# Optimization experiments

Hardware: AMD Instinct MI355X
Metric: run time of the kernel (lower is better)

The kernel has to match this reference:

```python
import jax, jax.numpy as jnp
import numpy as np

D_HEAD = 64

def setup_inputs() -> dict:
    key = jax.random.key(0)
    kq, kk, kv, km = jax.random.split(key, 4)
    B, H, S, D = 4, 16, 2048, D_HEAD
    q = jax.random.normal(kq, (B, H, S, D), dtype=jnp.float32)
    k = jax.random.normal(kk, (B, H, S, D), dtype=jnp.float32)
    v = jax.random.normal(kv, (B, H, S, D), dtype=jnp.float32)
    mask = jax.random.randint(km, (B, 1, S, S), 0, 2, dtype=jnp.int32)
    return {"q": q, "k": k, "v": v, "mask": mask}

def reference(q, k, v, mask):
    # scores: [B,H,S,S]
    scores = jnp.einsum('bhqd,bhkd->bhqk', q, k) / jnp.sqrt(jnp.asarray(D_HEAD, q.dtype))
    neg_inf = jnp.asarray(-jnp.inf, scores.dtype)
    scores = jnp.where(mask == 0, neg_inf, scores)
    attn = jax.nn.softmax(scores, axis=-1)
    # dropout is identity in eval mode (deterministic reference)
    return jnp.einsum('bhqk,bhkd->bhqd', attn, v)
```

## Files before the change

kernel.cpp:

```cpp
#include <hip/hip_runtime.h>


constexpr int Bc = 4, Hc = 16, Sc = 2048, Dc = 64;
constexpr int QBLK = 128, KVBLK = 64;
constexpr int NT = Sc / KVBLK;

typedef _Float16 half8 __attribute__((ext_vector_type(8)));
typedef _Float16 half4 __attribute__((ext_vector_type(4)));
typedef _Float16 half2v __attribute__((ext_vector_type(2)));
typedef __fp16  fp16x2 __attribute__((ext_vector_type(2)));
typedef float floatx4 __attribute__((ext_vector_type(4)));

#define GLB(p) ((const __attribute__((address_space(1))) void*)(p))
#define LDSP(p) ((__attribute__((address_space(3))) void*)(p))

union U32F2 { unsigned int u; fp16x2 h; };
union U32H2 { unsigned int u; half2v h; };
union PFRAG { unsigned int u[4]; half8 h; };

__device__ inline float dot2acc(unsigned int pu, float acc) {
#if __has_builtin(__builtin_amdgcn_fdot2)
    U32H2 c; c.u = pu;
    half2v ones2 = { (_Float16)1.0f, (_Float16)1.0f };
    return __builtin_amdgcn_fdot2(c.h, ones2, acc, false);
#else
    U32H2 c; c.u = pu;
    return acc + (float)c.h[0] + (float)c.h[1];
#endif
}

__global__ __launch_bounds__(256) void mask_to_bits(
    const int* __restrict__ M, unsigned long long* __restrict__ W)
{
    size_t i = (size_t)blockIdx.x * 256 + threadIdx.x;
    int v = M[i];
    unsigned long long bal = __ballot(v != 0);
    if ((threadIdx.x & 63) == 0) W[i >> 6] = bal;
}

__global__ __launch_bounds__(256) void mask_to_bytes(
    const int* __restrict__ M, unsigned int* __restrict__ M8)
{
    size_t t = (size_t)blockIdx.x * 256 + threadIdx.x;
    const int4* src = (const int4*)M + t * 4;
    uint4 out;
    unsigned int* o = (unsigned int*)&out;
    #pragma unroll
    for (int w = 0; w < 4; ++w) {
        int4 v = src[w];
        o[w] = (v.x ? 0xFFu : 0u) | (v.y ? 0xFF00u : 0u) |
               (v.z ? 0xFF0000u : 0u) | (v.w ? 0xFF000000u : 0u);
    }
    ((uint4*)M8)[t] = out;
}

__global__ __launch_bounds__(256) void kv_convert_v4(
    const float* __restrict__ Kp, const float* __restrict__ Vp,
    unsigned char* __restrict__ K16, unsigned char* __restrict__ V16)
{
    __shared__ float vlds[64][65];
    const int tid = threadIdx.x;
    const int kt  = blockIdx.x;
    const int bh  = blockIdx.y;
    const int kv0 = kt * 64;
    const float* ksrc = Kp + ((size_t)bh * Sc + kv0) * Dc;
    const float* vsrc = Vp + ((size_t)bh * Sc + kv0) * Dc;
    unsigned char* kdst = K16 + (size_t)bh * Sc * 128 + (size_t)kv0 * 128;
    unsigned char* vdst = V16 + (size_t)bh * Sc * 128 + (size_t)kv0 * 128;

    #pragma unroll
    for (int it = 0; it < 4; ++it) {
        int idx = it * 256 + tid;
        int o   = idx >> 4;
        int d0  = (idx & 15) * 4;
        float4 kval = *(const float4*)(ksrc + o * Dc + d0);
        half4 kh;
        kh[0] = (_Float16)kval.x; kh[1] = (_Float16)kval.y;
        kh[2] = (_Float16)kval.z; kh[3] = (_Float16)kval.w;
        int r = ((o >> 2) & 3) * 16 + ((o >> 4) << 2) + (o & 3);
        *(half4*)(kdst + r * 128 + ((d0 * 2) ^ ((r & 7) << 4))) = kh;

        float4 vval = *(const float4*)(vsrc + o * Dc + d0);
        vlds[o][d0]     = vval.x;
        vlds[o][d0 + 1] = vval.y;
        vlds[o][d0 + 2] = vval.z;
        vlds[o][d0 + 3] = vval.w;
    }
    __syncthreads();
    #pragma unroll
    for (int i = 0; i < 2; ++i) {
        int ch  = i * 256 + tid;
        int l15 = ch & 15;
        int lg  = (ch >> 4) & 3;
        int c   = (ch >> 6) & 1;
        int nd  = ch >> 7;
        int d   = nd * 16 + l15;
        half8 h;
        #pragma unroll
        for (int w = 0; w < 4; ++w) {
            int kvlog = lg * 16 + (2 * c + (w >> 1)) * 4 + (w & 1) * 2;
            h[w * 2]     = (_Float16)vlds[kvlog][d];
            h[w * 2 + 1] = (_Float16)vlds[kvlog + 1][d];
        }
        *(half8*)(vdst + ch * 16) = h;
    }
}

template <int MMODE>
__global__ __launch_bounds__(256) void attn_v10(
    const float* __restrict__ Qp,
    const unsigned char* __restrict__ K16, const unsigned char* __restrict__ V16,
    const unsigned char* __restrict__ M8, const unsigned long long* __restrict__ Wb,
    float* __restrict__ Op)
{
    __shared__ __align__(16) unsigned char lds[49152];

    const int tid  = threadIdx.x;
    const int w    = tid >> 6;
    const int lane = tid & 63;
    const int l15  = lane & 15;
    const int lg   = lane >> 4;

    const int ib      = blockIdx.x;
    const int logical = (ib & 7) * 128 + (ib >> 3);
    const int qt = logical & 15;
    const int bh = logical >> 4;
    const int b  = bh >> 4;
    const int q0 = qt * QBLK + w * 32 + l15;
    const int q1 = q0 + 16;

    const size_t qkv_base = (size_t)bh * Sc * Dc;
    const unsigned char* k16src = K16 + (size_t)bh * Sc * 128;
    const unsigned char* v16src = V16 + (size_t)bh * Sc * 128;
    const unsigned char* mp0 = M8 + (size_t)b * Sc * Sc + (size_t)q0 * Sc + lg * 16;
    const unsigned char* mp1 = mp0 + (size_t)16 * Sc;
    const unsigned long long* wr0 = Wb + ((size_t)b * Sc + q0) * (Sc / 64);
    const unsigned long long* wr1 = Wb + ((size_t)b * Sc + q1) * (Sc / 64);

    const float qscale = 0.125f * 1.44269504088896f;
    half8 qfrag[2][2];
    #pragma unroll
    for (int qg = 0; qg < 2; ++qg) {
        const float* qrow = Qp + qkv_base + (size_t)(qg ? q1 : q0) * Dc;
        #pragma unroll
        for (int c = 0; c < 2; ++c) {
            int d0 = c * 32 + lg * 8;
            float4 qa = *(const float4*)(qrow + d0);
            float4 qb = *(const float4*)(qrow + d0 + 4);
            qfrag[qg][c][0] = (_Float16)(qa.x * qscale);
            qfrag[qg][c][1] = (_Float16)(qa.y * qscale);
            qfrag[qg][c][2] = (_Float16)(qa.z * qscale);
            qfrag[qg][c][3] = (_Float16)(qa.w * qscale);
            qfrag[qg][c][4] = (_Float16)(qb.x * qscale);
            qfrag[qg][c][5] = (_Float16)(qb.y * qscale);
            qfrag[qg][c][6] = (_Float16)(qb.z * qscale);
            qfrag[qg][c][7] = (_Float16)(qb.w * qscale);
        }
    }

    floatx4 o_acc[2][4];
    float   l_run[2] = {0.f, 0.f};
    #pragma unroll
    for (int qg = 0; qg < 2; ++qg)
        #pragma unroll
        for (int n = 0; n < 4; ++n) o_acc[qg][n] = (floatx4)0.f;

    const int ldsOff = (w * 2) * 1024;
    const unsigned char* kg = k16src + ldsOff + lane * 16;
    const unsigned char* vg = v16src + ldsOff + lane * 16;

    uint4 mk[3][2];
    unsigned long long wk[3][2];

    auto STAGE = [&](int slot) {
        __builtin_amdgcn_global_load_lds(GLB(kg),        LDSP(lds + slot * 16384 + ldsOff),               16, 0, 0);
        __builtin_amdgcn_global_load_lds(GLB(kg + 1024), LDSP(lds + slot * 16384 + ldsOff + 1024),        16, 0, 0);
        __builtin_amdgcn_global_load_lds(GLB(vg),        LDSP(lds + slot * 16384 + 8192 + ldsOff),        16, 0, 0);
        __builtin_amdgcn_global_load_lds(GLB(vg + 1024), LDSP(lds + slot * 16384 + 8192 + ldsOff + 1024), 16, 0, 0);
        kg += 8192; vg += 8192;
    };
    auto LOADM = [&](int slot) {
        if (MMODE == 0) {
            mk[slot][0] = *(const uint4*)(mp0); mp0 += KVBLK;
            mk[slot][1] = *(const uint4*)(mp1); mp1 += KVBLK;
        } else {
            wk[slot][0] = *wr0; ++wr0;
            wk[slot][1] = *wr1; ++wr1;
        }
    };

    auto COMP = [&](int j) {
        const unsigned char* kbase = lds + j * 16384;
        const unsigned char* vbase = lds + j * 16384 + 8192;

        floatx4 s[2][4];
        __builtin_amdgcn_s_setprio(1);
        #pragma unroll
        for (int n = 0; n < 4; ++n) {
            const unsigned char* krow = kbase + (n * 16 + l15) * 128;
            half8 kf0 = *(const half8*)(krow + ((lg * 16)      ^ ((l15 & 7) << 4)));
            half8 kf1 = *(const half8*)(krow + ((64 + lg * 16) ^ ((l15 & 7) << 4)));
            floatx4 a0 = __builtin_amdgcn_mfma_f32_16x16x32_f16(kf0, qfrag[0][0], (floatx4)0.f, 0, 0, 0);
            a0 = __builtin_amdgcn_mfma_f32_16x16x32_f16(kf1, qfrag[0][1], a0, 0, 0, 0);
            floatx4 a1 = __builtin_amdgcn_mfma_f32_16x16x32_f16(kf0, qfrag[1][0], (floatx4)0.f, 0, 0, 0);
            a1 = __builtin_amdgcn_mfma_f32_16x16x32_f16(kf1, qfrag[1][1], a1, 0, 0, 0);
            s[0][n] = a0;
            s[1][n] = a1;
        }
        __builtin_amdgcn_s_setprio(0);

        PFRAG pf[2][2];
        #pragma unroll
        for (int qg = 0; qg < 2; ++qg) {
            unsigned int nib16;
            if (MMODE == 1) {
                unsigned long long wc = wk[j][qg];
                unsigned int lo = (unsigned int)wc, hi = (unsigned int)(wc >> 32);
                unsigned int half = (lg & 2) ? hi : lo;
                nib16 = (lg & 1) ? (half >> 16) : (half & 0xFFFFu);
            }
            const unsigned int* mw = (const unsigned int*)&mk[j][qg];
            float rs = l_run[qg];
            #pragma unroll
            for (int n = 0; n < 4; ++n) {
                float p0 = __builtin_amdgcn_exp2f(s[qg][n][0]);
                float p1 = __builtin_amdgcn_exp2f(s[qg][n][1]);
                float p2 = __builtin_amdgcn_exp2f(s[qg][n][2]);
                float p3 = __builtin_amdgcn_exp2f(s[qg][n][3]);
                U32F2 h01, h23;
                h01.h = __builtin_amdgcn_cvt_pkrtz(p0, p1);
                h23.h = __builtin_amdgcn_cvt_pkrtz(p2, p3);
                unsigned int msk0, msk1;
                if (MMODE == 0) {
                    msk0 = __builtin_amdgcn_perm(0u, mw[n], 0x01010000u);
                    msk1 = __builtin_amdgcn_perm(0u, mw[n], 0x03030202u);
                } else {
                    unsigned int x0 = nib16 >> (n * 4);
                    unsigned int x1 = nib16 >> (n * 4 + 2);
                    msk0 = ((x0 & 1u) | ((x0 & 2u) << 15)) * 0xFFFFu;
                    msk1 = ((x1 & 1u) | ((x1 & 2u) << 15)) * 0xFFFFu;
                }
                unsigned int w0 = h01.u & msk0;
                unsigned int w1 = h23.u & msk1;
                pf[qg][n >> 1].u[(n & 1) * 2]     = w0;
                pf[qg][n >> 1].u[(n & 1) * 2 + 1] = w1;
                rs = dot2acc(w0, rs);
                rs = dot2acc(w1, rs);
            }
            l_run[qg] = rs;
        }

        __builtin_amdgcn_s_setprio(1);
        #pragma unroll
        for (int nd = 0; nd < 4; ++nd) {
            const unsigned char* vrow = vbase + ((nd * 8 + lg) * 16 + l15) * 16;
            half8 vf0 = *(const half8*)(vrow);
            half8 vf1 = *(const half8*)(vrow + 1024);
            o_acc[0][nd] = __builtin_amdgcn_mfma_f32_16x16x32_f16(vf0, pf[0][0].h, o_acc[0][nd], 0, 0, 0);
            o_acc[0][nd] = __builtin_amdgcn_mfma_f32_16x16x32_f16(vf1, pf[0][1].h, o_acc[0][nd], 0, 0, 0);
            o_acc[1][nd] = __builtin_amdgcn_mfma_f32_16x16x32_f16(vf0, pf[1][0].h, o_acc[1][nd], 0, 0, 0);
            o_acc[1][nd] = __builtin_amdgcn_mfma_f32_16x16x32_f16(vf1, pf[1][1].h, o_acc[1][nd], 0, 0, 0);
        }
        __builtin_amdgcn_s_setprio(0);
    };

    STAGE(0); LOADM(0);
    STAGE(1); LOADM(1);

    for (int i = 0; i < 10; ++i) {
        #pragma unroll
        for (int j = 0; j < 3; ++j) {
            asm volatile("s_waitcnt vmcnt(6)" ::: "memory");
            __builtin_amdgcn_s_barrier();
            STAGE((j + 2) % 3);
            LOADM((j + 2) % 3);
            COMP(j);
        }
    }
    asm volatile("s_waitcnt vmcnt(6)" ::: "memory");
    __builtin_amdgcn_s_barrier();
    COMP(0);
    asm volatile("s_waitcnt vmcnt(0)" ::: "memory");
    __builtin_amdgcn_s_barrier();
    COMP(1);

    #pragma unroll
    for (int qg = 0; qg < 2; ++qg) {
        float r = l_run[qg];
        r += __shfl_xor(r, 16);
        r += __shfl_xor(r, 32);
        float inv_l = 1.0f / r;
        float* orow = Op + qkv_base + (size_t)(qg ? q1 : q0) * Dc;
        #pragma unroll
        for (int nd = 0; nd < 4; ++nd) {
            float4 st;
            st.x = o_acc[qg][nd][0] * inv_l;
            st.y = o_acc[qg][nd][1] * inv_l;
            st.z = o_acc[qg][nd][2] * inv_l;
            st.w = o_acc[qg][nd][3] * inv_l;
            *(float4*)(orow + nd * 16 + lg * 4) = st;
        }
    }
}

template <bool USE_BITS>
__global__ __launch_bounds__(256) void attn_old(
    const float* __restrict__ Qp, const float* __restrict__ Kp,
    const float* __restrict__ Vp, const int* __restrict__ Mp,
    const unsigned long long* __restrict__ Wb, float* __restrict__ Op)
{
    __shared__ __align__(16) unsigned char lds[24576];
    const int tid  = threadIdx.x;
    const int w    = tid >> 6;
    const int lane = tid & 63;
    const int l15  = lane & 15;
    const int lg   = lane >> 4;
    const int qt = blockIdx.x;
    const int bh = blockIdx.y;
    const int b  = bh >> 4;
    const int qbase = qt * 64;
    const size_t qkv_base = (size_t)bh * Sc * Dc;
    const int*   mrow     = Mp + (size_t)b * Sc * Sc;
    const unsigned long long* wrow =
        Wb + ((size_t)b * Sc + qbase + w * 16 + lg * 4) * (Sc / 64);

    const float qscale = 0.125f * 1.44269504088896f;
    half8 qfrag[2];
    {
        const float* qrow = Qp + qkv_base + (size_t)(qbase + w * 16 + l15) * Dc;
        #pragma unroll
        for (int c = 0; c < 2; ++c) {
            int d0 = c * 32 + lg * 8;
            float4 qa = *(const float4*)(qrow + d0);
            float4 qb = *(const float4*)(qrow + d0 + 4);
            #pragma unroll
            for (int e = 0; e < 4; ++e) qfrag[c][e] = (_Float16)(((const float*)&qa)[e] * qscale);
            #pragma unroll
            for (int e = 0; e < 4; ++e) qfrag[c][4 + e] = (_Float16)(((const float*)&qb)[e] * qscale);
        }
    }
    float m_run[4], l_run[4];
    floatx4 o_acc[4];
    #pragma unroll
    for (int j = 0; j < 4; ++j) { m_run[j] = -1e30f; l_run[j] = 0.f; }
    #pragma unroll
    for (int n = 0; n < 4; ++n) o_acc[n] = (floatx4)0.f;

    for (int kv0 = 0; kv0 < Sc; kv0 += 64) {
        __syncthreads();
        {
            const float* ksrc = Kp + qkv_base + (size_t)kv0 * Dc;
            const float* vsrc = Vp + qkv_base + (size_t)kv0 * Dc;
            #pragma unroll
            for (int it = 0; it < 4; ++it) {
                int idx = it * 256 + tid;
                int kv  = idx >> 4;
                int d0  = (idx & 15) * 4;
                float4 kval = *(const float4*)(ksrc + kv * Dc + d0);
                half4 kh;
                kh[0] = (_Float16)kval.x; kh[1] = (_Float16)kval.y;
                kh[2] = (_Float16)kval.z; kh[3] = (_Float16)kval.w;
                *(half4*)(lds + ((kv * 128 + d0 * 2) ^ ((kv & 7) << 4))) = kh;
                float4 vval = *(const float4*)(vsrc + kv * Dc + d0);
                float vv[4] = { vval.x, vval.y, vval.z, vval.w };
                #pragma unroll
                for (int i = 0; i < 4; ++i) {
                    int d = d0 + i;
                    *(_Float16*)(lds + 8192 + ((d * 128 + kv * 2) ^ ((d & 7) << 4))) = (_Float16)vv[i];
                }
            }
        }
        __syncthreads();

        unsigned int mlo[4], mhi[4];
        if (USE_BITS) {
            #pragma unroll
            for (int j = 0; j < 4; ++j) {
                unsigned long long mw = wrow[(size_t)j * (Sc / 64) + (kv0 >> 6)];
                mlo[j] = (unsigned int)mw;
                mhi[j] = (unsigned int)(mw >> 32);
            }
        }
        floatx4 s[4];
        #pragma unroll
        for (int n = 0; n < 4; ++n) {
            floatx4 acc = (floatx4)0.f;
            #pragma unroll
            for (int c = 0; c < 2; ++c) {
                int kvr = n * 16 + l15;
                int d0  = c * 32 + lg * 8;
                half8 bfrag = *(const half8*)(lds + ((kvr * 128 + d0 * 2) ^ ((kvr & 7) << 4)));
                acc = __builtin_amdgcn_mfma_f32_16x16x32_f16(qfrag[c], bfrag, acc, 0, 0, 0);
            }
            s[n] = acc;
        }
        float tmax[4];
        #pragma unroll
        for (int j = 0; j < 4; ++j) tmax[j] = -1e30f;
        #pragma unroll
        for (int n = 0; n < 4; ++n) {
            #pragma unroll
            for (int j = 0; j < 4; ++j) {
                unsigned int bit;
                if (USE_BITS) {
                    unsigned int word = (n < 2) ? mlo[j] : mhi[j];
                    bit = (word >> (((n & 1) << 4) + l15)) & 1u;
                } else {
                    int qr  = qbase + w * 16 + lg * 4 + j;
                    int kvc = kv0 + n * 16 + l15;
                    bit = (mrow[(size_t)qr * Sc + kvc] != 0) ? 1u : 0u;
                }
                float sv = bit ? s[n][j] : -1e30f;
                s[n][j] = sv;
                tmax[j] = fmaxf(tmax[j], sv);
            }
        }
        #pragma unroll
        for (int j = 0; j < 4; ++j) {
            float tv = tmax[j];
            tv = fmaxf(tv, __shfl_xor(tv, 1));
            tv = fmaxf(tv, __shfl_xor(tv, 2));
            tv = fmaxf(tv, __shfl_xor(tv, 4));
            tv = fmaxf(tv, __shfl_xor(tv, 8));
            tmax[j] = tv;
        }
        float corr[4], rsum[4];
        #pragma unroll
        for (int j = 0; j < 4; ++j) {
            float mnew = fmaxf(m_run[j], tmax[j]);
            corr[j] = exp2f(m_run[j] - mnew);
            m_run[j] = mnew;
            rsum[j] = 0.f;
        }
        unsigned char* pbase = lds + 16384 + w * 2048;
        #pragma unroll
        for (int n = 0; n < 4; ++n) {
            #pragma unroll
            for (int j = 0; j < 4; ++j) {
                float p = exp2f(s[n][j] - m_run[j]);
                rsum[j] += p;
                int off = ((lg * 4 + j) * 128 + (n * 16 + l15) * 2) ^ (((lg * 4 + j) & 7) << 4);
                *(_Float16*)(pbase + off) = (_Float16)p;
            }
        }
        #pragma unroll
        for (int j = 0; j < 4; ++j) {
            float r = rsum[j];
            r += __shfl_xor(r, 1);
            r += __shfl_xor(r, 2);
            r += __shfl_xor(r, 4);
            r += __shfl_xor(r, 8);
            l_run[j] = l_run[j] * corr[j] + r;
        }
        #pragma unroll
        for (int n = 0; n < 4; ++n)
            #pragma unroll
            for (int j = 0; j < 4; ++j)
                o_acc[n][j] *= corr[j];

        half8 pfrag[2];
        #pragma unroll
        for (int c = 0; c < 2; ++c) {
            int kvc = c * 32 + lg * 8;
            pfrag[c] = *(const half8*)(pbase + ((l15 * 128 + kvc * 2) ^ ((l15 & 7) << 4)));
        }
        #pragma unroll
        for (int n = 0; n < 4; ++n) {
            #pragma unroll
            for (int c = 0; c < 2; ++c) {
                int d   = n * 16 + l15;
                int kvc = c * 32 + lg * 8;
                half8 vfrag = *(const half8*)(lds + 8192 + ((d * 128 + kvc * 2) ^ ((d & 7) << 4)));
                o_acc[n] = __builtin_amdgcn_mfma_f32_16x16x32_f16(pfrag[c], vfrag, o_acc[n], 0, 0, 0);
            }
        }
    }
    float inv_l[4];
    #pragma unroll
    for (int j = 0; j < 4; ++j) inv_l[j] = 1.0f / l_run[j];
    float* obase = Op + qkv_base;
    #pragma unroll
    for (int n = 0; n < 4; ++n)
        #pragma unroll
        for (int j = 0; j < 4; ++j)
            obase[(size_t)(qbase + w * 16 + lg * 4 + j) * Dc + n * 16 + l15] = o_acc[n][j] * inv_l[j];
}

extern "C" void kernel_launch(void* const* d_in, const int* in_sizes, int n_in,
                              void* d_out, int out_size, void* d_ws, size_t ws_size,
                              hipStream_t stream) {
    const float* Q = (const float*)d_in[0];
    const float* K = (const float*)d_in[1];
    const float* V = (const float*)d_in[2];
    const int*   M = (const int*)d_in[3];
    float*       O = (float*)d_out;

    const int nblk = (Sc / QBLK) * Bc * Hc;
    const size_t SZ_BITS = (size_t)Bc * Sc * (Sc / 64) * 8;
    const size_t SZ_K    = (size_t)Bc * Hc * Sc * 128;
    const size_t SZ_V    = SZ_K;
    const size_t SZ_M8   = (size_t)Bc * Sc * Sc;

    if (ws_size >= SZ_K + SZ_V + SZ_M8) {
        unsigned char* K16 = (unsigned char*)d_ws;
        unsigned char* V16 = K16 + SZ_K;
        unsigned char* M8  = V16 + SZ_V;
        mask_to_bytes<<<(Bc * Sc * Sc) / (256 * 16), 256, 0, stream>>>(M, (unsigned int*)M8);
        kv_convert_v4<<<dim3(Sc / 64, Bc * Hc), 256, 0, stream>>>(K, V, K16, V16);
        attn_v10<0><<<nblk, 256, 0, stream>>>(Q, K16, V16, M8, nullptr, O);
    } else if (ws_size >= SZ_BITS + SZ_K + SZ_V) {
        unsigned long long* W = (unsigned long long*)d_ws;
        unsigned char* K16 = (unsigned char*)d_ws + SZ_BITS;
        unsigned char* V16 = K16 + SZ_K;
        mask_to_bits<<<(Bc * Sc * Sc) / 256, 256, 0, stream>>>(M, W);
        kv_convert_v4<<<dim3(Sc / 64, Bc * Hc), 256, 0, stream>>>(K, V, K16, V16);
        attn_v10<1><<<nblk, 256, 0, stream>>>(Q, K16, V16, nullptr, W, O);
    } else if (ws_size >= SZ_BITS) {
        unsigned long long* W = (unsigned long long*)d_ws;
        mask_to_bits<<<(Bc * Sc * Sc) / 256, 256, 0, stream>>>(M, W);
        attn_old<true><<<dim3(Sc / 64, Bc * Hc), 256, 0, stream>>>(Q, K, V, M, W, O);
    } else {
        attn_old<false><<<dim3(Sc / 64, Bc * Hc), 256, 0, stream>>>(Q, K, V, M, nullptr, O);
    }
}
```

Measured before the change: 125.4 us.

## Load K/V fragments directly from global memory instead of LDS-staged triple buffer

Removes the 48KB shared-memory triple-buffered async staging of K and V tiles, along with its barriers and waitcnt pipeline. Each wave now loads its MFMA K/V fragments straight from global memory, which relies on L1/L2 to serve the redundant reads across the four waves. Mask loads move inline per tile. The aim is to drop LDS pressure and block-wide synchronisation, likely raising occupancy. The cost is duplicated global traffic and exposed load latency without explicit prefetch.

Result: slower. 141.6 us (+12.9%).

```diff
diff --git a/kernel.cpp b/kernel.cpp
--- a/kernel.cpp
+++ b/kernel.cpp
@@ -10,9 +10,6 @@
 typedef _Float16 half2v __attribute__((ext_vector_type(2)));
 typedef __fp16  fp16x2 __attribute__((ext_vector_type(2)));
 typedef float floatx4 __attribute__((ext_vector_type(4)));
-
-#define GLB(p) ((const __attribute__((address_space(1))) void*)(p))
-#define LDSP(p) ((__attribute__((address_space(3))) void*)(p))
 
 union U32F2 { unsigned int u; fp16x2 h; };
 union U32H2 { unsigned int u; half2v h; };
@@ -107,14 +104,12 @@
 }
 
 template <int MMODE>
-__global__ __launch_bounds__(256) void attn_v10(
+__global__ __launch_bounds__(256) void attn_v12(
     const float* __restrict__ Qp,
     const unsigned char* __restrict__ K16, const unsigned char* __restrict__ V16,
     const unsigned char* __restrict__ M8, const unsigned long long* __restrict__ Wb,
     float* __restrict__ Op)
 {
-    __shared__ __align__(16) unsigned char lds[49152];
-
     const int tid  = threadIdx.x;
     const int w    = tid >> 6;
     const int lane = tid & 63;
@@ -130,12 +125,14 @@
     const int q1 = q0 + 16;
 
     const size_t qkv_base = (size_t)bh * Sc * Dc;
-    const unsigned char* k16src = K16 + (size_t)bh * Sc * 128;
-    const unsigned char* v16src = V16 + (size_t)bh * Sc * 128;
     const unsigned char* mp0 = M8 + (size_t)b * Sc * Sc + (size_t)q0 * Sc + lg * 16;
     const unsigned char* mp1 = mp0 + (size_t)16 * Sc;
     const unsigned long long* wr0 = Wb + ((size_t)b * Sc + q0) * (Sc / 64);
     const unsigned long long* wr1 = Wb + ((size_t)b * Sc + q1) * (Sc / 64);
+
+    const unsigned char* kp0 = K16 + (size_t)bh * Sc * 128 + l15 * 128 + ((lg * 16)      ^ ((l15 & 7) << 4));
+    const unsigned char* kp1 = K16 + (size_t)bh * Sc * 128 + l15 * 128 + ((64 + lg * 16) ^ ((l15 & 7) << 4));
+    const unsigned char* vp  = V16 + (size_t)bh * Sc * 128 + (lg * 16 + l15) * 16;
 
     const float qscale = 0.125f * 1.44269504088896f;
     half8 qfrag[2][2];
@@ -165,61 +162,44 @@
         #pragma unroll
         for (int n = 0; n < 4; ++n) o_acc[qg][n] = (floatx4)0.f;
 
-    const int ldsOff = (w * 2) * 1024;
-    const unsigned char* kg = k16src + ldsOff + lane * 16;
-    const unsigned char* vg = v16src + ldsOff + lane * 16;
-
-    uint4 mk[3][2];
-    unsigned long long wk[3][2];
-
-    auto STAGE = [&](int slot) {
-        __builtin_amdgcn_global_load_lds(GLB(kg),        LDSP(lds + slot * 16384 + ldsOff),               16, 0, 0);
-        __builtin_amdgcn_global_load_lds(GLB(kg + 1024), LDSP(lds + slot * 16384 + ldsOff + 1024),        16, 0, 0);
-        __builtin_amdgcn_global_load_lds(GLB(vg),        LDSP(lds + slot * 16384 + 8192 + ldsOff),        16, 0, 0);
-        __builtin_amdgcn_global_load_lds(GLB(vg + 1024), LDSP(lds + slot * 16384 + 8192 + ldsOff + 1024), 16, 0, 0);
-        kg += 8192; vg += 8192;
-    };
-    auto LOADM = [&](int slot) {
-        if (MMODE == 0) {
-            mk[slot][0] = *(const uint4*)(mp0); mp0 += KVBLK;
-            mk[slot][1] = *(const uint4*)(mp1); mp1 += KVBLK;
-        } else {
-            wk[slot][0] = *wr0; ++wr0;
-            wk[slot][1] = *wr1; ++wr1;
-        }
-    };
-
-    auto COMP = [&](int j) {
-        const unsigned char* kbase = lds + j * 16384;
-        const unsigned char* vbase = lds + j * 16384 + 8192;
-
+    for (int t = 0; t < NT; ++t) {
         floatx4 s[2][4];
-        __builtin_amdgcn_s_setprio(1);
         #pragma unroll
         for (int n = 0; n < 4; ++n) {
-            const unsigned char* krow = kbase + (n * 16 + l15) * 128;
-            half8 kf0 = *(const half8*)(krow + ((lg * 16)      ^ ((l15 & 7) << 4)));
-            half8 kf1 = *(const half8*)(krow + ((64 + lg * 16) ^ ((l15 & 7) << 4)));
+            half8 kf0 = *(const half8*)(kp0 + n * 2048);
+            half8 kf1 = *(const half8*)(kp1 + n * 2048);
+            __builtin_amdgcn_s_setprio(1);
             floatx4 a0 = __builtin_amdgcn_mfma_f32_16x16x32_f16(kf0, qfrag[0][0], (floatx4)0.f, 0, 0, 0);
             a0 = __builtin_amdgcn_mfma_f32_16x16x32_f16(kf1, qfrag[0][1], a0, 0, 0, 0);
             floatx4 a1 = __builtin_amdgcn_mfma_f32_16x16x32_f16(kf0, qfrag[1][0], (floatx4)0.f, 0, 0, 0);
             a1 = __builtin_amdgcn_mfma_f32_16x16x32_f16(kf1, qfrag[1][1], a1, 0, 0, 0);
+            __builtin_amdgcn_s_setprio(0);
             s[0][n] = a0;
             s[1][n] = a1;
         }
-        __builtin_amdgcn_s_setprio(0);
+        kp0 += 8192; kp1 += 8192;
+
+        uint4 mk0, mk1;
+        unsigned long long wk0, wk1;
+        if (MMODE == 0) {
+            mk0 = *(const uint4*)(mp0 + t * KVBLK);
+            mk1 = *(const uint4*)(mp1 + t * KVBLK);
+        } else {
+            wk0 = wr0[t];
+            wk1 = wr1[t];
+        }
 
         PFRAG pf[2][2];
         #pragma unroll
         for (int qg = 0; qg < 2; ++qg) {
             unsigned int nib16;
             if (MMODE == 1) {
-                unsigned long long wc = wk[j][qg];
+                unsigned long long wc = qg ? wk1 : wk0;
                 unsigned int lo = (unsigned int)wc, hi = (unsigned int)(wc >> 32);
                 unsigned int half = (lg & 2) ? hi : lo;
                 nib16 = (lg & 1) ? (half >> 16) : (half & 0xFFFFu);
             }
-            const unsigned int* mw = (const unsigned int*)&mk[j][qg];
+            const unsigned int* mw = (const unsigned int*)(qg ? &mk1 : &mk0);
             float rs = l_run[qg];
             #pragma unroll
             for (int n = 0; n < 4; ++n) {
@@ -250,39 +230,19 @@
             l_run[qg] = rs;
         }
 
-        __builtin_amdgcn_s_setprio(1);
         #pragma unroll
         for (int nd = 0; nd < 4; ++nd) {
-            const unsigned char* vrow = vbase + ((nd * 8 + lg) * 16 + l15) * 16;
-            half8 vf0 = *(const half8*)(vrow);
-            half8 vf1 = *(const half8*)(vrow + 1024);
+            half8 vf0 = *(const half8*)(vp + nd * 2048);
+            half8 vf1 = *(const half8*)(vp + nd * 2048 + 1024);
+            __builtin_amdgcn_s_setprio(1);
             o_acc[0][nd] = __builtin_amdgcn_mfma_f32_16x16x32_f16(vf0, pf[0][0].h, o_acc[0][nd], 0, 0, 0);
             o_acc[0][nd] = __builtin_amdgcn_mfma_f32_16x16x32_f16(vf1, pf[0][1].h, o_acc[0][nd], 0, 0, 0);
             o_acc[1][nd] = __builtin_amdgcn_mfma_f32_16x16x32_f16(vf0, pf[1][0].h, o_acc[1][nd], 0, 0, 0);
             o_acc[1][nd] = __builtin_amdgcn_mfma_f32_16x16x32_f16(vf1, pf[1][1].h, o_acc[1][nd], 0, 0, 0);
-        }
-        __builtin_amdgcn_s_setprio(0);
-    };
-
-    STAGE(0); LOADM(0);
-    STAGE(1); LOADM(1);
-
-    for (int i = 0; i < 10; ++i) {
-        #pragma unroll
-        for (int j = 0; j < 3; ++j) {
-            asm volatile("s_waitcnt vmcnt(6)" ::: "memory");
-            __builtin_amdgcn_s_barrier();
-            STAGE((j + 2) % 3);
-            LOADM((j + 2) % 3);
-            COMP(j);
-        }
-    }
-    asm volatile("s_waitcnt vmcnt(6)" ::: "memory");
-    __builtin_amdgcn_s_barrier();
-    COMP(0);
-    asm volatile("s_waitcnt vmcnt(0)" ::: "memory");
-    __builtin_amdgcn_s_barrier();
-    COMP(1);
+            __builtin_amdgcn_s_setprio(0);
+        }
+        vp += 8192;
+    }
 
     #pragma unroll
     for (int qg = 0; qg < 2; ++qg) {
@@ -507,14 +467,14 @@
         unsigned char* M8  = V16 + SZ_V;
         mask_to_bytes<<<(Bc * Sc * Sc) / (256 * 16), 256, 0, stream>>>(M, (unsigned int*)M8);
         kv_convert_v4<<<dim3(Sc / 64, Bc * Hc), 256, 0, stream>>>(K, V, K16, V16);
-        attn_v10<0><<<nblk, 256, 0, stream>>>(Q, K16, V16, M8, nullptr, O);
+        attn_v12<0><<<nblk, 256, 0, stream>>>(Q, K16, V16, M8, nullptr, O);
     } else if (ws_size >= SZ_BITS + SZ_K + SZ_V) {
         unsigned long long* W = (unsigned long long*)d_ws;
         unsigned char* K16 = (unsigned char*)d_ws + SZ_BITS;
         unsigned char* V16 = K16 + SZ_K;
         mask_to_bits<<<(Bc * Sc * Sc) / 256, 256, 0, stream>>>(M, W);
         kv_convert_v4<<<dim3(Sc / 64, Bc * Hc), 256, 0, stream>>>(K, V, K16, V16);
-        attn_v10<1><<<nblk, 256, 0, stream>>>(Q, K16, V16, nullptr, W, O);
+        attn_v12<1><<<nblk, 256, 0, stream>>>(Q, K16, V16, nullptr, W, O);
     } else if (ws_size >= SZ_BITS) {
         unsigned long long* W = (unsigned long long*)d_ws;
         mask_to_bits<<<(Bc * Sc * Sc) / 256, 256, 0, stream>>>(M, W);
```
